# Optimization experiments

Measured on AMD Instinct MI355X. Metric: run time of the kernel, lower is better.

The kernel has to match this reference:

```python
import jax, jax.numpy as jnp
import numpy as np

B, C, H, W = 4, 64, 64, 64


def setup_inputs() -> dict:
    key = jax.random.key(0)
    k1, k2, k3, k4, k5 = jax.random.split(key, 5)
    return {
        "x": jax.random.normal(k1, (B, C, H, W), dtype=jnp.float32),
        "w_qkv": jax.random.normal(k2, (3 * C, C), dtype=jnp.float32) * (1.0 / np.sqrt(C)),
        "b_qkv": jax.random.normal(k3, (3 * C,), dtype=jnp.float32) * 0.02,
        "w_proj": jax.random.normal(k4, (C, C), dtype=jnp.float32) * (1.0 / np.sqrt(C)),
        "b_proj": jax.random.normal(k5, (C,), dtype=jnp.float32) * 0.02,
    }


def reference(x, w_qkv, b_qkv, w_proj, b_proj):
    b, c, h, w = x.shape
    xf = x.reshape(b, c, h * w)                                  # [B, C, N]
    # 1x1 Conv1d == per-position linear over channels
    qkv = jnp.einsum('oc,bcn->bon', w_qkv, xf) + b_qkv[None, :, None]  # [B, 3C, N]
    q, k, v = jnp.split(qkv, 3, axis=1)                          # each [B, C, N]
    scores = jnp.einsum('bcn,bcm->bnm', q, k) / (c ** 0.5)       # [B, N, N]
    attn = jax.nn.softmax(scores, axis=-1)
    out = jnp.einsum('bcm,bnm->bcn', v, attn)                    # [B, C, N]
    out = jnp.einsum('oc,bcn->bon', w_proj, out) + b_proj[None, :, None]
    return out.reshape(b, c, h, w) + x
```

## Files before the change

### kernel.cpp

```cpp
#include <hip/hip_runtime.h>

typedef __bf16 bf16x8 __attribute__((ext_vector_type(8)));
typedef __bf16 bf16x4 __attribute__((ext_vector_type(4)));
typedef float f32x4 __attribute__((ext_vector_type(4)));
typedef short s16x4 __attribute__((ext_vector_type(4)));

#define NB 4
#define NC 64
#define NN 4096
#define SPLIT 8

#define QSCALE (0.125f * 1.44269504088896340736f)

#if __has_builtin(__builtin_amdgcn_exp2f)
#define EXP2(x) __builtin_amdgcn_exp2f(x)
#else
#define EXP2(x) exp2f(x)
#endif

__global__ __launch_bounds__(256) void qkv_kernel(
    const float* __restrict__ x, const float* __restrict__ wqkv,
    const float* __restrict__ bqkv,
    __bf16* __restrict__ Qg, __bf16* __restrict__ Kg, __bf16* __restrict__ Vg)
{
  const int tid = threadIdx.x;
  const int wave = tid >> 6;
  const int lane = tid & 63;
  const int quad = lane >> 4;
  const int l16 = lane & 15;
  const int b = blockIdx.y;
  const int tsel = blockIdx.z;
  const int n0 = blockIdx.x * 128 + wave * 32;
  const float wscale = (tsel == 0) ? QSCALE : 1.0f;

  bf16x8 wf[4][2];
#pragma unroll
  for (int ot = 0; ot < 4; ot++) {
#pragma unroll
    for (int ch = 0; ch < 2; ch++) {
      const float* wp =
          wqkv + (size_t)(tsel * 64 + ot * 16 + l16) * 64 + ch * 32 + quad * 8;
      const float4 w0 = *(const float4*)wp;
      const float4 w1 = *(const float4*)(wp + 4);
      bf16x8 f;
      f[0] = (__bf16)(w0.x * wscale); f[1] = (__bf16)(w0.y * wscale);
      f[2] = (__bf16)(w0.z * wscale); f[3] = (__bf16)(w0.w * wscale);
      f[4] = (__bf16)(w1.x * wscale); f[5] = (__bf16)(w1.y * wscale);
      f[6] = (__bf16)(w1.z * wscale); f[7] = (__bf16)(w1.w * wscale);
      wf[ot][ch] = f;
    }
  }
  float bv[4];
#pragma unroll
  for (int ot = 0; ot < 4; ot++)
    bv[ot] = bqkv[tsel * 64 + ot * 16 + l16] * wscale;

#pragma unroll
  for (int nt = 0; nt < 2; nt++) {
    const int nb = n0 + nt * 16 + l16;

    bf16x8 xf[2];
#pragma unroll
    for (int ch = 0; ch < 2; ch++) {
      float v[8];
#pragma unroll
      for (int j = 0; j < 8; j++)
        v[j] = x[(size_t)(b * 64 + ch * 32 + quad * 8 + j) * NN + nb];
      bf16x8 f;
#pragma unroll
      for (int j = 0; j < 8; j++) f[j] = (__bf16)v[j];
      xf[ch] = f;
    }

#pragma unroll
    for (int ot = 0; ot < 4; ot++) {
      f32x4 acc = (f32x4){bv[ot], bv[ot], bv[ot], bv[ot]};
      acc = __builtin_amdgcn_mfma_f32_16x16x32_bf16(xf[0], wf[ot][0], acc, 0, 0, 0);
      acc = __builtin_amdgcn_mfma_f32_16x16x32_bf16(xf[1], wf[ot][1], acc, 0, 0, 0);

      if (tsel < 2) {
        __bf16* dst = (tsel == 0) ? Qg : Kg;
#pragma unroll
        for (int r = 0; r < 4; r++)
          dst[(size_t)(b * NN + n0 + nt * 16 + quad * 4 + r) * 64 + ot * 16 + l16] =
              (__bf16)acc[r];
      } else {
        bf16x4 pv;
#pragma unroll
        for (int r = 0; r < 4; r++) pv[r] = (__bf16)acc[r];
        *(bf16x4*)(Vg + (size_t)(b * 64 + ot * 16 + l16) * NN +
                   n0 + nt * 16 + quad * 4) = pv;
      }
    }
  }
}

__global__ __launch_bounds__(256) void flash_kernel(
    const __bf16* __restrict__ Q, const __bf16* __restrict__ K,
    const __bf16* __restrict__ V, const float* __restrict__ wproj,
    __bf16* __restrict__ Opart, float* __restrict__ lpart)
{
  const int b = blockIdx.y;
  const int s = blockIdx.z;
  const int tid = threadIdx.x;
  const int wave = tid >> 6;
  const int lane = tid & 63;
  const int quad = lane >> 4;
  const int l16 = lane & 15;

  __shared__ __bf16 Kt[64 * 72];
  __shared__ __bf16 Vt[64 * 72];

  const int q0 = blockIdx.x * 128 + wave * 32;

  bf16x8 qf[2][2];
#pragma unroll
  for (int qt = 0; qt < 2; qt++) {
    const __bf16* qrow = Q + ((size_t)(b * NN + q0 + qt * 16 + l16)) * 64;
    qf[qt][0] = *(const bf16x8*)(qrow + quad * 8);
    qf[qt][1] = *(const bf16x8*)(qrow + 32 + quad * 8);
  }

  f32x4 acc[2][4];
#pragma unroll
  for (int qt = 0; qt < 2; qt++)
#pragma unroll
    for (int ct = 0; ct < 4; ct++) acc[qt][ct] = (f32x4){0.f, 0.f, 0.f, 0.f};
  float l[2] = {0.f, 0.f};

  const int kbeg = s * (NN / SPLIT);
  const int kend = kbeg + (NN / SPLIT);
#pragma unroll 1
  for (int kt0 = kbeg; kt0 < kend; kt0 += 64) {
    __syncthreads();
#pragma unroll
    for (int it = 0; it < 2; it++) {
      const int chunk = tid + it * 256;
      const int row = chunk >> 3, col8 = (chunk & 7) * 8;
      *(bf16x8*)(&Kt[row * 72 + col8]) =
          *(const bf16x8*)(K + ((size_t)(b * NN + kt0 + row)) * 64 + col8);
      *(bf16x8*)(&Vt[row * 72 + col8]) =
          *(const bf16x8*)(V + ((size_t)(b * 64 + row)) * NN + kt0 + col8);
    }
    __syncthreads();

    s16x4 pk[4][2];
#pragma unroll
    for (int t = 0; t < 4; t++) {
      const bf16x8 kf0 = *(const bf16x8*)(&Kt[(t * 16 + l16) * 72 + quad * 8]);
      const bf16x8 kf1 = *(const bf16x8*)(&Kt[(t * 16 + l16) * 72 + 32 + quad * 8]);
#pragma unroll
      for (int qt = 0; qt < 2; qt++) {
        f32x4 z = (f32x4){0.f, 0.f, 0.f, 0.f};
        z = __builtin_amdgcn_mfma_f32_16x16x32_bf16(kf0, qf[qt][0], z, 0, 0, 0);
        z = __builtin_amdgcn_mfma_f32_16x16x32_bf16(kf1, qf[qt][1], z, 0, 0, 0);
        const float p0 = EXP2(z[0]), p1 = EXP2(z[1]);
        const float p2 = EXP2(z[2]), p3 = EXP2(z[3]);
        l[qt] += (p0 + p1) + (p2 + p3);
        bf16x4 pv;
        pv[0] = (__bf16)p0; pv[1] = (__bf16)p1;
        pv[2] = (__bf16)p2; pv[3] = (__bf16)p3;
        pk[t][qt] = __builtin_bit_cast(s16x4, pv);
      }
    }

#pragma unroll
    for (int kg = 0; kg < 4; kg++) {
#pragma unroll
      for (int ct = 0; ct < 4; ct++) {
        const bf16x4 va =
            *(const bf16x4*)(&Vt[(ct * 16 + l16) * 72 + kg * 16 + quad * 4]);
        const s16x4 a = __builtin_bit_cast(s16x4, va);
        acc[0][ct] = __builtin_amdgcn_mfma_f32_16x16x16bf16_1k(
            a, pk[kg][0], acc[0][ct], 0, 0, 0);
        acc[1][ct] = __builtin_amdgcn_mfma_f32_16x16x16bf16_1k(
            a, pk[kg][1], acc[1][ct], 0, 0, 0);
      }
    }
  }

#pragma unroll
  for (int qt = 0; qt < 2; qt++) {
    float lr = l[qt];
    lr += __shfl_xor(lr, 16);
    lr += __shfl_xor(lr, 32);
    if (quad == 0)
      lpart[((size_t)(s * NB + b)) * NN + q0 + qt * 16 + l16] = lr;
  }

  s16x4 ob[2][4];
#pragma unroll
  for (int qt = 0; qt < 2; qt++)
#pragma unroll
    for (int ch = 0; ch < 4; ch++) {
      bf16x4 t;
#pragma unroll
      for (int r = 0; r < 4; r++) t[r] = (__bf16)acc[qt][ch][r];
      ob[qt][ch] = __builtin_bit_cast(s16x4, t);
    }

#pragma unroll
  for (int cot = 0; cot < 4; cot++) {
    f32x4 po[2];
    po[0] = (f32x4){0.f, 0.f, 0.f, 0.f};
    po[1] = (f32x4){0.f, 0.f, 0.f, 0.f};
#pragma unroll
    for (int ch = 0; ch < 4; ch++) {
      const float4 wv =
          *(const float4*)&wproj[(cot * 16 + l16) * 64 + ch * 16 + quad * 4];
      bf16x4 wb;
      wb[0] = (__bf16)wv.x; wb[1] = (__bf16)wv.y;
      wb[2] = (__bf16)wv.z; wb[3] = (__bf16)wv.w;
      const s16x4 a = __builtin_bit_cast(s16x4, wb);
      po[0] = __builtin_amdgcn_mfma_f32_16x16x16bf16_1k(a, ob[0][ch], po[0], 0, 0, 0);
      po[1] = __builtin_amdgcn_mfma_f32_16x16x16bf16_1k(a, ob[1][ch], po[1], 0, 0, 0);
    }
#pragma unroll
    for (int qt = 0; qt < 2; qt++)
#pragma unroll
      for (int r = 0; r < 4; r++)
        Opart[(((size_t)(s * NB + b)) * 64 + cot * 16 + quad * 4 + r) * NN +
              q0 + qt * 16 + l16] = (__bf16)po[qt][r];
  }
}

__global__ __launch_bounds__(256) void combine_kernel(
    const __bf16* __restrict__ Opart, const float* __restrict__ lpart,
    const float* __restrict__ bproj, const float* __restrict__ x,
    float* __restrict__ out)
{
  const int b = blockIdx.y;
  const int n0 = blockIdx.x * 32;
  const int tid = threadIdx.x;

  __shared__ float linv[32];
  if (tid < 32) {
    float lt = 0.f;
#pragma unroll
    for (int s = 0; s < SPLIT; s++)
      lt += lpart[((size_t)(s * NB + b)) * NN + n0 + tid];
    linv[tid] = 1.0f / lt;
  }
  __syncthreads();

  const int c = tid >> 2;
  const int n8 = (tid & 3) * 8;

  float o[8];
#pragma unroll
  for (int j = 0; j < 8; j++) o[j] = 0.f;
#pragma unroll
  for (int s = 0; s < SPLIT; s++) {
    const bf16x8 v = *(const bf16x8*)(
        Opart + (((size_t)(s * NB + b)) * 64 + c) * NN + n0 + n8);
#pragma unroll
    for (int j = 0; j < 8; j++) o[j] += (float)v[j];
  }

  const float bb = bproj[c];
  const float4 li0 = *(const float4*)&linv[n8];
  const float4 li1 = *(const float4*)&linv[n8 + 4];
  const size_t base = ((size_t)(b * 64 + c)) * NN + n0 + n8;
  const float4 x0 = *(const float4*)&x[base];
  const float4 x1 = *(const float4*)&x[base + 4];
  float4 r0, r1;
  r0.x = o[0] * li0.x + bb + x0.x;  r0.y = o[1] * li0.y + bb + x0.y;
  r0.z = o[2] * li0.z + bb + x0.z;  r0.w = o[3] * li0.w + bb + x0.w;
  r1.x = o[4] * li1.x + bb + x1.x;  r1.y = o[5] * li1.y + bb + x1.y;
  r1.z = o[6] * li1.z + bb + x1.z;  r1.w = o[7] * li1.w + bb + x1.w;
  *(float4*)&out[base] = r0;
  *(float4*)&out[base + 4] = r1;
}

extern "C" void kernel_launch(void* const* d_in, const int* in_sizes, int n_in,
                              void* d_out, int out_size, void* d_ws, size_t ws_size,
                              hipStream_t stream) {
  const float* x     = (const float*)d_in[0];
  const float* wqkv  = (const float*)d_in[1];
  const float* bqkv  = (const float*)d_in[2];
  const float* wproj = (const float*)d_in[3];
  const float* bproj = (const float*)d_in[4];
  float* out = (float*)d_out;

  char* ws = (char*)d_ws;
  __bf16* Q     = (__bf16*)(ws);
  __bf16* K     = (__bf16*)(ws + (2u << 20));
  __bf16* V     = (__bf16*)(ws + (4u << 20));
  __bf16* Opart = (__bf16*)(ws + (6u << 20));
  float*  lpart = (float*)(ws + (23u << 20));

  qkv_kernel<<<dim3(32, NB, 3), 256, 0, stream>>>(x, wqkv, bqkv, Q, K, V);
  flash_kernel<<<dim3(32, NB, SPLIT), 256, 0, stream>>>(Q, K, V, wproj,
                                                        Opart, lpart);
  combine_kernel<<<dim3(128, NB), 256, 0, stream>>>(Opart, lpart, bproj, x,
                                                    out);
}
```

Before: 114.3 us.

## Double-buffer K/V tiles via direct global-to-LDS loads with XOR swizzle

Replaces the register-staged K/V tile copy in the flash kernel with global_load_lds (direct to LDS) into two ping-pong buffers. The next tile is prefetched while the current one is consumed, which drops one barrier per iteration. Padding is replaced by an XOR swizzle of 16-byte chunks to avoid LDS bank conflicts. This doubles LDS usage, which may lower occupancy. It also relies on the asynchronous LDS loads being complete at the single barrier, and there is no explicit vmcnt wait, so ordering is a correctness risk.

```diff
diff --git a/kernel.cpp b/kernel.cpp
--- a/kernel.cpp
+++ b/kernel.cpp
@@ -17,6 +17,11 @@
 #else
 #define EXP2(x) exp2f(x)
 #endif
+
+#define GLL16(src, dst)                                                  \
+  __builtin_amdgcn_global_load_lds(                                      \
+      (const __attribute__((address_space(1))) void*)(src),              \
+      (__attribute__((address_space(3))) void*)(dst), 16, 0, 0)
 
 __global__ __launch_bounds__(256) void qkv_kernel(
     const float* __restrict__ x, const float* __restrict__ wqkv,
@@ -108,8 +113,8 @@
   const int quad = lane >> 4;
   const int l16 = lane & 15;
 
-  __shared__ __bf16 Kt[64 * 72];
-  __shared__ __bf16 Vt[64 * 72];
+  __shared__ __bf16 KB[2][64 * 64];
+  __shared__ __bf16 VB[2][64 * 64];
 
   const int q0 = blockIdx.x * 128 + wave * 32;
 
@@ -121,6 +126,32 @@
     qf[qt][1] = *(const bf16x8*)(qrow + 32 + quad * 8);
   }
 
+  const int h = l16 & 7;
+  const int ko0 = (quad ^ h) << 3;
+  const int ko1 = ((quad + 4) ^ h) << 3;
+  int vo[4];
+#pragma unroll
+  for (int kg = 0; kg < 4; kg++)
+    vo[kg] = ((((kg << 1) + (quad >> 1)) ^ h) << 3) + ((quad & 1) << 2);
+
+  const int c0 = wave * 128 + lane;
+  const int c1 = c0 + 64;
+  const int r0 = c0 >> 3, r1 = c1 >> 3;
+  const int k0 = (c0 & 7) ^ (r0 & 7);
+  const int k1 = (c1 & 7) ^ (r1 & 7);
+  const int kbeg = s * (NN / SPLIT);
+  const __bf16* Ks0 = K + ((size_t)b * NN + kbeg + r0) * 64 + k0 * 8;
+  const __bf16* Ks1 = K + ((size_t)b * NN + kbeg + r1) * 64 + k1 * 8;
+  const __bf16* Vs0 = V + ((size_t)(b * 64 + r0)) * NN + kbeg + k0 * 8;
+  const __bf16* Vs1 = V + ((size_t)(b * 64 + r1)) * NN + kbeg + k1 * 8;
+  const int db0 = wave * 128 * 8;
+  const int db1 = db0 + 64 * 8;
+
+  GLL16(Ks0, &KB[0][db0]);
+  GLL16(Ks1, &KB[0][db1]);
+  GLL16(Vs0, &VB[0][db0]);
+  GLL16(Vs1, &VB[0][db1]);
+
   f32x4 acc[2][4];
 #pragma unroll
   for (int qt = 0; qt < 2; qt++)
@@ -128,27 +159,30 @@
     for (int ct = 0; ct < 4; ct++) acc[qt][ct] = (f32x4){0.f, 0.f, 0.f, 0.f};
   float l[2] = {0.f, 0.f};
 
-  const int kbeg = s * (NN / SPLIT);
-  const int kend = kbeg + (NN / SPLIT);
+  __syncthreads();
+
+  const int NT = (NN / SPLIT) / 64;
+  int cur = 0;
 #pragma unroll 1
-  for (int kt0 = kbeg; kt0 < kend; kt0 += 64) {
-    __syncthreads();
-#pragma unroll
-    for (int it = 0; it < 2; it++) {
-      const int chunk = tid + it * 256;
-      const int row = chunk >> 3, col8 = (chunk & 7) * 8;
-      *(bf16x8*)(&Kt[row * 72 + col8]) =
-          *(const bf16x8*)(K + ((size_t)(b * NN + kt0 + row)) * 64 + col8);
-      *(bf16x8*)(&Vt[row * 72 + col8]) =
-          *(const bf16x8*)(V + ((size_t)(b * 64 + row)) * NN + kt0 + col8);
-    }
-    __syncthreads();
+  for (int t8 = 0; t8 < NT; t8++) {
+    if (t8 + 1 < NT) {
+      const int nb = cur ^ 1;
+      const size_t kadv = (size_t)(t8 + 1) * 64 * 64;
+      const int vadv = (t8 + 1) * 64;
+      GLL16(Ks0 + kadv, &KB[nb][db0]);
+      GLL16(Ks1 + kadv, &KB[nb][db1]);
+      GLL16(Vs0 + vadv, &VB[nb][db0]);
+      GLL16(Vs1 + vadv, &VB[nb][db1]);
+    }
+    const __bf16* Kb = KB[cur];
+    const __bf16* Vb = VB[cur];
 
     s16x4 pk[4][2];
 #pragma unroll
     for (int t = 0; t < 4; t++) {
-      const bf16x8 kf0 = *(const bf16x8*)(&Kt[(t * 16 + l16) * 72 + quad * 8]);
-      const bf16x8 kf1 = *(const bf16x8*)(&Kt[(t * 16 + l16) * 72 + 32 + quad * 8]);
+      const __bf16* krow = Kb + (t * 16 + l16) * 64;
+      const bf16x8 kf0 = *(const bf16x8*)(krow + ko0);
+      const bf16x8 kf1 = *(const bf16x8*)(krow + ko1);
 #pragma unroll
       for (int qt = 0; qt < 2; qt++) {
         f32x4 z = (f32x4){0.f, 0.f, 0.f, 0.f};
@@ -169,7 +203,7 @@
 #pragma unroll
       for (int ct = 0; ct < 4; ct++) {
         const bf16x4 va =
-            *(const bf16x4*)(&Vt[(ct * 16 + l16) * 72 + kg * 16 + quad * 4]);
+            *(const bf16x4*)(Vb + (ct * 16 + l16) * 64 + vo[kg]);
         const s16x4 a = __builtin_bit_cast(s16x4, va);
         acc[0][ct] = __builtin_amdgcn_mfma_f32_16x16x16bf16_1k(
             a, pk[kg][0], acc[0][ct], 0, 0, 0);
@@ -177,6 +211,9 @@
             a, pk[kg][1], acc[1][ct], 0, 0, 0);
       }
     }
+
+    if (t8 + 1 < NT) __syncthreads();
+    cur ^= 1;
   }
 
 #pragma unroll
```

After: 113.7 us. No clear change (-0.6%).

## Rework flash kernel with 32x32 MFMA, async LDS double buffering and swizzle

Applied to the files above, without the earlier changes.

The flash attention kernel moves from 16x16 MFMA tiles to 32x32x16 bf16 MFMAs and stages K/V tiles with global_load_lds into double-buffered, XOR-swizzled shared memory, so the next tile loads while the current one computes. Softmax probabilities are repacked into B operands with v_permlane32_swap instead of separate 16x16 fragments. The projection epilogue also uses 32x32 MFMAs. This aims to cut LDS bank conflicts, load latency and per-MFMA instruction overhead. In exchange it adds register pressure from the 16-wide accumulators under launch_bounds(256,4) and relies on lane-layout assumptions that must be exactly right.

```diff
diff --git a/kernel.cpp b/kernel.cpp
--- a/kernel.cpp
+++ b/kernel.cpp
@@ -2,8 +2,11 @@
 
 typedef __bf16 bf16x8 __attribute__((ext_vector_type(8)));
 typedef __bf16 bf16x4 __attribute__((ext_vector_type(4)));
+typedef __bf16 bf16x2 __attribute__((ext_vector_type(2)));
 typedef float f32x4 __attribute__((ext_vector_type(4)));
+typedef float f32x16 __attribute__((ext_vector_type(16)));
 typedef short s16x4 __attribute__((ext_vector_type(4)));
+typedef unsigned int u32x4 __attribute__((ext_vector_type(4)));
 
 #define NB 4
 #define NC 64
@@ -17,6 +20,11 @@
 #else
 #define EXP2(x) exp2f(x)
 #endif
+
+#define GLL16(src, dst)                                                  \
+  __builtin_amdgcn_global_load_lds(                                      \
+      (const __attribute__((address_space(1))) void*)(src),              \
+      (__attribute__((address_space(3))) void*)(dst), 16, 0, 0)
 
 __global__ __launch_bounds__(256) void qkv_kernel(
     const float* __restrict__ x, const float* __restrict__ wqkv,
@@ -95,7 +103,7 @@
   }
 }
 
-__global__ __launch_bounds__(256) void flash_kernel(
+__global__ __launch_bounds__(256, 4) void flash_kernel(
     const __bf16* __restrict__ Q, const __bf16* __restrict__ K,
     const __bf16* __restrict__ V, const float* __restrict__ wproj,
     __bf16* __restrict__ Opart, float* __restrict__ lpart)
@@ -105,123 +113,156 @@
   const int tid = threadIdx.x;
   const int wave = tid >> 6;
   const int lane = tid & 63;
-  const int quad = lane >> 4;
-  const int l16 = lane & 15;
-
-  __shared__ __bf16 Kt[64 * 72];
-  __shared__ __bf16 Vt[64 * 72];
+  const int l32 = lane & 31;
+  const int h = lane >> 5;
+
+  __shared__ __bf16 KB[2][64 * 64];
+  __shared__ __bf16 VB[2][64 * 64];
 
   const int q0 = blockIdx.x * 128 + wave * 32;
 
-  bf16x8 qf[2][2];
-#pragma unroll
-  for (int qt = 0; qt < 2; qt++) {
-    const __bf16* qrow = Q + ((size_t)(b * NN + q0 + qt * 16 + l16)) * 64;
-    qf[qt][0] = *(const bf16x8*)(qrow + quad * 8);
-    qf[qt][1] = *(const bf16x8*)(qrow + 32 + quad * 8);
-  }
-
-  f32x4 acc[2][4];
-#pragma unroll
-  for (int qt = 0; qt < 2; qt++)
-#pragma unroll
-    for (int ct = 0; ct < 4; ct++) acc[qt][ct] = (f32x4){0.f, 0.f, 0.f, 0.f};
-  float l[2] = {0.f, 0.f};
-
+  bf16x8 qf[4];
+  {
+    const __bf16* qrow = Q + ((size_t)(b * NN + q0 + l32)) * 64 + h * 8;
+    qf[0] = *(const bf16x8*)(qrow);
+    qf[1] = *(const bf16x8*)(qrow + 16);
+    qf[2] = *(const bf16x8*)(qrow + 32);
+    qf[3] = *(const bf16x8*)(qrow + 48);
+  }
+
+  int koff[4];
+#pragma unroll
+  for (int i = 0; i < 4; i++) koff[i] = ((2 * i + h) ^ (lane & 7)) << 3;
+
+  const int c0 = wave * 128 + lane;
+  const int c1 = c0 + 64;
+  const int r0 = c0 >> 3, r1 = c1 >> 3;
+  const int k0 = (c0 & 7) ^ (r0 & 7);
+  const int k1 = (c1 & 7) ^ (r1 & 7);
   const int kbeg = s * (NN / SPLIT);
-  const int kend = kbeg + (NN / SPLIT);
+  const __bf16* Ks0 = K + ((size_t)b * NN + kbeg + r0) * 64 + k0 * 8;
+  const __bf16* Ks1 = K + ((size_t)b * NN + kbeg + r1) * 64 + k1 * 8;
+  const __bf16* Vs0 = V + ((size_t)(b * 64 + r0)) * NN + kbeg + k0 * 8;
+  const __bf16* Vs1 = V + ((size_t)(b * 64 + r1)) * NN + kbeg + k1 * 8;
+  const int db0 = wave * 1024;
+  const int db1 = db0 + 512;
+
+#define STAGE(BUF, T)                                                    \
+  {                                                                      \
+    GLL16(Ks0 + (size_t)(T) * 4096, &KB[BUF][db0]);                      \
+    GLL16(Ks1 + (size_t)(T) * 4096, &KB[BUF][db1]);                      \
+    GLL16(Vs0 + (T) * 64, &VB[BUF][db0]);                                \
+    GLL16(Vs1 + (T) * 64, &VB[BUF][db1]);                                \
+  }
+
+  f32x16 oacc[2] = {};
+  float l = 0.f;
+
+  STAGE(0, 0);
+  __syncthreads();
+
+#define TILE_COMPUTE(BUF)                                                \
+  {                                                                      \
+    u32x4 bw[4];                                                         \
+    _Pragma("unroll")                                                    \
+    for (int kg = 0; kg < 2; kg++) {                                     \
+      f32x16 sa = {};                                                    \
+      _Pragma("unroll")                                                  \
+      for (int cs = 0; cs < 4; cs++) {                                   \
+        const bf16x8 kf =                                                \
+            *(const bf16x8*)(&KB[BUF][(kg * 32 + l32) * 64 + koff[cs]]); \
+        sa = __builtin_amdgcn_mfma_f32_32x32x16_bf16(kf, qf[cs], sa, 0, 0, 0); \
+      }                                                                  \
+      _Pragma("unroll")                                                  \
+      for (int i = 0; i < 16; i++) sa[i] = EXP2(sa[i]);                  \
+      l += ((sa[0] + sa[1]) + (sa[2] + sa[3])) +                         \
+           ((sa[4] + sa[5]) + (sa[6] + sa[7])) +                         \
+           ((sa[8] + sa[9]) + (sa[10] + sa[11])) +                       \
+           ((sa[12] + sa[13]) + (sa[14] + sa[15]));                      \
+      unsigned w[8];                                                     \
+      _Pragma("unroll")                                                  \
+      for (int i = 0; i < 8; i++) {                                      \
+        bf16x2 t2;                                                       \
+        t2[0] = (__bf16)sa[2 * i]; t2[1] = (__bf16)sa[2 * i + 1];        \
+        w[i] = __builtin_bit_cast(unsigned, t2);                         \
+      }                                                                  \
+      asm("v_permlane32_swap_b32 %0, %1" : "+v"(w[0]), "+v"(w[2]));      \
+      asm("v_permlane32_swap_b32 %0, %1" : "+v"(w[1]), "+v"(w[3]));      \
+      asm("v_permlane32_swap_b32 %0, %1" : "+v"(w[4]), "+v"(w[6]));      \
+      asm("v_permlane32_swap_b32 %0, %1" : "+v"(w[5]), "+v"(w[7]));      \
+      bw[kg * 2]     = (u32x4){w[0], w[1], w[2], w[3]};                  \
+      bw[kg * 2 + 1] = (u32x4){w[4], w[5], w[6], w[7]};                  \
+    }                                                                    \
+    _Pragma("unroll")                                                    \
+    for (int cg = 0; cg < 2; cg++) {                                     \
+      _Pragma("unroll")                                                  \
+      for (int ks = 0; ks < 4; ks++) {                                   \
+        const bf16x8 va =                                                \
+            *(const bf16x8*)(&VB[BUF][(cg * 32 + l32) * 64 + koff[ks]]); \
+        oacc[cg] = __builtin_amdgcn_mfma_f32_32x32x16_bf16(              \
+            va, __builtin_bit_cast(bf16x8, bw[ks]), oacc[cg], 0, 0, 0);  \
+      }                                                                  \
+    }                                                                    \
+  }
+
+  const int NT = (NN / SPLIT) / 64;
 #pragma unroll 1
-  for (int kt0 = kbeg; kt0 < kend; kt0 += 64) {
+  for (int t = 0; t < NT; t += 2) {
+    if (t + 1 < NT) STAGE(1, t + 1);
+    TILE_COMPUTE(0);
     __syncthreads();
-#pragma unroll
-    for (int it = 0; it < 2; it++) {
-      const int chunk = tid + it * 256;
-      const int row = chunk >> 3, col8 = (chunk & 7) * 8;
-      *(bf16x8*)(&Kt[row * 72 + col8]) =
-          *(const bf16x8*)(K + ((size_t)(b * NN + kt0 + row)) * 64 + col8);
-      *(bf16x8*)(&Vt[row * 72 + col8]) =
-          *(const bf16x8*)(V + ((size_t)(b * 64 + row)) * NN + kt0 + col8);
-    }
-    __syncthreads();
-
-    s16x4 pk[4][2];
-#pragma unroll
-    for (int t = 0; t < 4; t++) {
-      const bf16x8 kf0 = *(const bf16x8*)(&Kt[(t * 16 + l16) * 72 + quad * 8]);
-      const bf16x8 kf1 = *(const bf16x8*)(&Kt[(t * 16 + l16) * 72 + 32 + quad * 8]);
-#pragma unroll
-      for (int qt = 0; qt < 2; qt++) {
-        f32x4 z = (f32x4){0.f, 0.f, 0.f, 0.f};
-        z = __builtin_amdgcn_mfma_f32_16x16x32_bf16(kf0, qf[qt][0], z, 0, 0, 0);
-        z = __builtin_amdgcn_mfma_f32_16x16x32_bf16(kf1, qf[qt][1], z, 0, 0, 0);
-        const float p0 = EXP2(z[0]), p1 = EXP2(z[1]);
-        const float p2 = EXP2(z[2]), p3 = EXP2(z[3]);
-        l[qt] += (p0 + p1) + (p2 + p3);
-        bf16x4 pv;
-        pv[0] = (__bf16)p0; pv[1] = (__bf16)p1;
-        pv[2] = (__bf16)p2; pv[3] = (__bf16)p3;
-        pk[t][qt] = __builtin_bit_cast(s16x4, pv);
-      }
-    }
-
-#pragma unroll
-    for (int kg = 0; kg < 4; kg++) {
-#pragma unroll
-      for (int ct = 0; ct < 4; ct++) {
-        const bf16x4 va =
-            *(const bf16x4*)(&Vt[(ct * 16 + l16) * 72 + kg * 16 + quad * 4]);
-        const s16x4 a = __builtin_bit_cast(s16x4, va);
-        acc[0][ct] = __builtin_amdgcn_mfma_f32_16x16x16bf16_1k(
-            a, pk[kg][0], acc[0][ct], 0, 0, 0);
-        acc[1][ct] = __builtin_amdgcn_mfma_f32_16x16x16bf16_1k(
-            a, pk[kg][1], acc[1][ct], 0, 0, 0);
-      }
-    }
-  }
-
-#pragma unroll
-  for (int qt = 0; qt < 2; qt++) {
-    float lr = l[qt];
-    lr += __shfl_xor(lr, 16);
-    lr += __shfl_xor(lr, 32);
-    if (quad == 0)
-      lpart[((size_t)(s * NB + b)) * NN + q0 + qt * 16 + l16] = lr;
-  }
-
-  s16x4 ob[2][4];
-#pragma unroll
-  for (int qt = 0; qt < 2; qt++)
-#pragma unroll
-    for (int ch = 0; ch < 4; ch++) {
-      bf16x4 t;
-#pragma unroll
-      for (int r = 0; r < 4; r++) t[r] = (__bf16)acc[qt][ch][r];
-      ob[qt][ch] = __builtin_bit_cast(s16x4, t);
-    }
-
-#pragma unroll
-  for (int cot = 0; cot < 4; cot++) {
-    f32x4 po[2];
-    po[0] = (f32x4){0.f, 0.f, 0.f, 0.f};
-    po[1] = (f32x4){0.f, 0.f, 0.f, 0.f};
-#pragma unroll
-    for (int ch = 0; ch < 4; ch++) {
-      const float4 wv =
-          *(const float4*)&wproj[(cot * 16 + l16) * 64 + ch * 16 + quad * 4];
-      bf16x4 wb;
-      wb[0] = (__bf16)wv.x; wb[1] = (__bf16)wv.y;
-      wb[2] = (__bf16)wv.z; wb[3] = (__bf16)wv.w;
-      const s16x4 a = __builtin_bit_cast(s16x4, wb);
-      po[0] = __builtin_amdgcn_mfma_f32_16x16x16bf16_1k(a, ob[0][ch], po[0], 0, 0, 0);
-      po[1] = __builtin_amdgcn_mfma_f32_16x16x16bf16_1k(a, ob[1][ch], po[1], 0, 0, 0);
-    }
-#pragma unroll
-    for (int qt = 0; qt < 2; qt++)
-#pragma unroll
-      for (int r = 0; r < 4; r++)
-        Opart[(((size_t)(s * NB + b)) * 64 + cot * 16 + quad * 4 + r) * NN +
-              q0 + qt * 16 + l16] = (__bf16)po[qt][r];
-  }
+    if (t + 2 < NT) STAGE(0, t + 2);
+    TILE_COMPUTE(1);
+    if (t + 2 < NT) __syncthreads();
+  }
+
+  l += __shfl_xor(l, 32);
+  if (h == 0)
+    lpart[((size_t)(s * NB + b)) * NN + q0 + l32] = l;
+
+  u32x4 ow[4];
+#pragma unroll
+  for (int cg = 0; cg < 2; cg++) {
+    unsigned w[8];
+#pragma unroll
+    for (int i = 0; i < 8; i++) {
+      bf16x2 t2;
+      t2[0] = (__bf16)oacc[cg][2 * i]; t2[1] = (__bf16)oacc[cg][2 * i + 1];
+      w[i] = __builtin_bit_cast(unsigned, t2);
+    }
+    asm("v_permlane32_swap_b32 %0, %1" : "+v"(w[0]), "+v"(w[2]));
+    asm("v_permlane32_swap_b32 %0, %1" : "+v"(w[1]), "+v"(w[3]));
+    asm("v_permlane32_swap_b32 %0, %1" : "+v"(w[4]), "+v"(w[6]));
+    asm("v_permlane32_swap_b32 %0, %1" : "+v"(w[5]), "+v"(w[7]));
+    ow[cg * 2]     = (u32x4){w[0], w[1], w[2], w[3]};
+    ow[cg * 2 + 1] = (u32x4){w[4], w[5], w[6], w[7]};
+  }
+
+#pragma unroll
+  for (int cog = 0; cog < 2; cog++) {
+    f32x16 po = {};
+#pragma unroll
+    for (int cs = 0; cs < 4; cs++) {
+      const float* wp = wproj + (size_t)(cog * 32 + l32) * 64 + cs * 16 + h * 8;
+      const float4 w0 = *(const float4*)wp;
+      const float4 w1 = *(const float4*)(wp + 4);
+      bf16x8 wa;
+      wa[0] = (__bf16)w0.x; wa[1] = (__bf16)w0.y;
+      wa[2] = (__bf16)w0.z; wa[3] = (__bf16)w0.w;
+      wa[4] = (__bf16)w1.x; wa[5] = (__bf16)w1.y;
+      wa[6] = (__bf16)w1.z; wa[7] = (__bf16)w1.w;
+      po = __builtin_amdgcn_mfma_f32_32x32x16_bf16(
+          wa, __builtin_bit_cast(bf16x8, ow[cs]), po, 0, 0, 0);
+    }
+#pragma unroll
+    for (int reg = 0; reg < 16; reg++) {
+      const int co = cog * 32 + (reg & 3) + 8 * (reg >> 2) + 4 * h;
+      Opart[(((size_t)(s * NB + b)) * 64 + co) * NN + q0 + l32] =
+          (__bf16)po[reg];
+    }
+  }
+#undef STAGE
+#undef TILE_COMPUTE
 }
 
 __global__ __launch_bounds__(256) void combine_kernel(
```

New measurement: 136.7 us. 1.2x slower.
